# Optimization experiments

Measured on AMD Instinct MI355X. Metric: run time of the kernel, lower is better.

The kernel has to match this reference:

```python
import jax, jax.numpy as jnp
import numpy as np
import math

B, N, D, H, BS = 1, 2048, 1024, 16, 256  # batch, seq, d_model, heads, block_size


def setup_inputs() -> dict:
    key = jax.random.key(0)
    ks = jax.random.split(key, 8)
    s = 0.02  # init scale for projection weights
    return {
        "x": jax.random.normal(ks[0], (B, N, D), jnp.float32),
        "distance_bias": jax.random.uniform(ks[1], (N, N), dtype=jnp.float32),
        "Wq": jax.random.normal(ks[2], (D, D), jnp.float32) * s,
        "bq": jnp.zeros((D,), jnp.float32),
        "Wk": jax.random.normal(ks[3], (D, D), jnp.float32) * s,
        "bk": jnp.zeros((D,), jnp.float32),
        "Wv": jax.random.normal(ks[4], (D, D), jnp.float32) * s,
        "bv": jnp.zeros((D,), jnp.float32),
        "Wo": jax.random.normal(ks[5], (D, D), jnp.float32) * s,
        "bo": jnp.zeros((D,), jnp.float32),
    }


def reference(x, distance_bias, Wq, bq, Wk, bk, Wv, bv, Wo, bo):
    Bm, Nm, Dm = x.shape
    dk = Dm // H
    scale = 1.0 / math.sqrt(dk)
    nb = Nm // BS  # number of blocks along sequence

    def proj(W, b):
        # torch Linear: x @ W.T + b, then split heads -> [B, H, N, dk]
        return (x @ W.T + b).reshape(Bm, Nm, H, dk).transpose(0, 2, 1, 3)

    Q, K, V = proj(Wq, bq), proj(Wk, bk), proj(Wv, bv)

    # scores with toroidal bias subtracted (matches `scores - bias_block`)
    scores = jnp.einsum('bhqd,bhkd->bhqk', Q, K) * scale - distance_bias[None, None]
    # view as [B, H, n_qblk, BS, n_kblk, BS] and softmax PER (q-block, k-block)
    s6 = scores.reshape(Bm, H, nb, BS, nb, BS)
    w = jax.nn.softmax(s6, axis=-1)  # softmax over keys within each kv block

    Vb = V.reshape(Bm, H, nb, BS, dk)
    # sum over all kv blocks of (per-block softmax) @ V_block
    num = jnp.einsum('bhqsnk,bhnkd->bhqsd', w, Vb)  # [B,H,nb,BS,dk]
    # accumulated normalizer = sum of per-block softmax weights over all kv blocks
    norm = jnp.sum(w, axis=(4, 5))  # [B,H,nb,BS]
    O = num / (norm[..., None] + 1e-8)

    O = O.reshape(Bm, H, Nm, dk).transpose(0, 2, 1, 3).reshape(Bm, Nm, Dm)
    return O @ Wo.T + bo
```

## Files before the change

### kernel.cpp

```cpp
#include <hip/hip_runtime.h>
#include <hip/hip_fp16.h>

typedef _Float16 half8 __attribute__((ext_vector_type(8)));
typedef _Float16 half4v __attribute__((ext_vector_type(4)));
typedef float f32x4 __attribute__((ext_vector_type(4)));

#define NSEQ 2048
#define DMOD 1024
#define NHEAD 16
#define DK 64

#define GLOAD_LDS16(gp, lp) __builtin_amdgcn_global_load_lds(                 \
    (const __attribute__((address_space(1))) void*)(gp),                      \
    (__attribute__((address_space(3))) void*)(lp), 16, 0, 0)

#define WAIT_VM(n) (0xF70 | (n))


__global__ __launch_bounds__(256) void cast_pack(
    const float* __restrict__ x, const float* __restrict__ wq,
    const float* __restrict__ wk, const float* __restrict__ wv,
    const float* __restrict__ wo, _Float16* __restrict__ dst)
{
    const int w = blockIdx.x * 4 + (threadIdx.x >> 6);
    const int ln = threadIdx.x & 63, m = ln & 15, qd = ln >> 4;
    const float* src; _Float16* d; int loc;
    if (w < 4096) { src = x; d = dst; loc = w; }
    else {
        const int w2 = w - 4096, mat = w2 >> 11;
        loc = w2 & 2047;
        src = mat == 0 ? wq : mat == 1 ? wk : mat == 2 ? wv : wo;
        d = dst + 2097152 + mat * 1048576;
    }
    const int st = loc >> 5, kc = loc & 31;
    const float* p = src + (size_t)(st * 16 + m) * 1024 + kc * 32 + qd * 8;
    float4 a = *(const float4*)p, b = *(const float4*)(p + 4);
    half8 h;
    h[0] = (_Float16)a.x; h[1] = (_Float16)a.y; h[2] = (_Float16)a.z; h[3] = (_Float16)a.w;
    h[4] = (_Float16)b.x; h[5] = (_Float16)b.y; h[6] = (_Float16)b.z; h[7] = (_Float16)b.w;
    *(half8*)(d + (size_t)(loc * 64 + ln) * 8) = h;
}

__global__ __launch_bounds__(256) void cvt_bias(
    const float* __restrict__ src, _Float16* __restrict__ dst)
{
    int i = (blockIdx.x * 256 + threadIdx.x) * 4;
    float4 v = *(const float4*)(src + i);
    half4v h;
    h[0] = (_Float16)v.x; h[1] = (_Float16)v.y;
    h[2] = (_Float16)v.z; h[3] = (_Float16)v.w;
    *(half4v*)(dst + i) = h;
}

__global__ __launch_bounds__(256) void combine(
    const _Float16* __restrict__ a, const _Float16* __restrict__ b,
    _Float16* __restrict__ o)
{
    int i = (blockIdx.x * 256 + threadIdx.x) * 8;
    half8 x = *(const half8*)(a + i);
    half8 y = *(const half8*)(b + i);
    half8 r;
#pragma unroll
    for (int j = 0; j < 8; ++j) r[j] = (_Float16)((float)x[j] + (float)y[j]);
    *(half8*)(o + i) = r;
}

template<int BM, int BN, int MODE>
__global__ __launch_bounds__(256) void tgemm(
    const _Float16* __restrict__ A,
    const _Float16* __restrict__ W0, const _Float16* __restrict__ W1,
    const _Float16* __restrict__ W2,
    const float* __restrict__ b0, const float* __restrict__ b1,
    const float* __restrict__ b2,
    _Float16* __restrict__ oQ, _Float16* __restrict__ oK,
    _Float16* __restrict__ oV, float* __restrict__ oF)
{
    constexpr int MT = BM / 32, NT = BN / 32;
    constexpr int NA = BM / 64, NB = BN / 64;
    __shared__ _Float16 sA[3 * BM * 32];
    __shared__ _Float16 sB[3 * BN * 32];
    const int tid = threadIdx.x, wv = tid >> 6, ln = tid & 63;
    const int m = ln & 15, qd = ln >> 4;
    const int row0 = blockIdx.x * BM;

    int sel = 0, colbase;
    const _Float16* W; const float* bias;
    if constexpr (MODE == 0) {
        sel = blockIdx.y >> 3;
        colbase = (blockIdx.y & 7) * BN;
        W = sel == 0 ? W0 : sel == 1 ? W1 : W2;
        bias = sel == 0 ? b0 : sel == 1 ? b1 : b2;
    } else {
        colbase = blockIdx.y * BN;
        W = W0; bias = b0;
    }
    const int wr = wv >> 1, wc = wv & 1;

    f32x4 acc[MT][NT];
#pragma unroll
    for (int i = 0; i < MT; ++i)
#pragma unroll
        for (int j = 0; j < NT; ++j) acc[i][j] = (f32x4){0.f, 0.f, 0.f, 0.f};

    auto stage = [&](int kc, int b) {
        _Float16* dA = sA + b * (BM * 32);
        _Float16* dB = sB + b * (BN * 32);
#pragma unroll
        for (int ra = 0; ra < NA; ++ra) {
            const int st = ra * 4 + wv;
            GLOAD_LDS16(A + ((size_t)((row0 >> 4) + st) * 32 + kc) * 512 + ln * 8,
                        dA + st * 512);
        }
#pragma unroll
        for (int rb = 0; rb < NB; ++rb) {
            const int st = rb * 4 + wv;
            GLOAD_LDS16(W + ((size_t)((colbase >> 4) + st) * 32 + kc) * 512 + ln * 8,
                        dB + st * 512);
        }
    };
    auto step = [&](int b) {
        const _Float16* cA = sA + b * (BM * 32);
        const _Float16* cB = sB + b * (BN * 32);
        half8 af[MT], bf[NT];
#pragma unroll
        for (int i = 0; i < MT; ++i)
            af[i] = *(const half8*)(cA + ((wr * MT + i) * 64 + ln) * 8);
#pragma unroll
        for (int j = 0; j < NT; ++j)
            bf[j] = *(const half8*)(cB + ((wc * NT + j) * 64 + ln) * 8);
#pragma unroll
        for (int i = 0; i < MT; ++i)
#pragma unroll
            for (int j = 0; j < NT; ++j)
                acc[i][j] = __builtin_amdgcn_mfma_f32_16x16x32_f16(af[i], bf[j], acc[i][j], 0, 0, 0);
    };

    stage(0, 0);
    stage(1, 1);
#pragma unroll
    for (int kc = 0; kc < 31; ++kc) {
        __builtin_amdgcn_s_waitcnt(WAIT_VM(NA + NB));
        __builtin_amdgcn_s_barrier();
        if (kc < 30) stage(kc + 2, (kc + 2) % 3);
        step(kc % 3);
    }
    __builtin_amdgcn_s_waitcnt(WAIT_VM(0));
    __builtin_amdgcn_s_barrier();
    step(1);

#pragma unroll
    for (int j = 0; j < NT; ++j) {
        const int col = colbase + wc * (BN / 2) + j * 16 + m;
        const float bv = bias[col];
#pragma unroll
        for (int i = 0; i < MT; ++i) {
            const int crow0 = row0 + wr * (BM / 2) + i * 16 + qd * 4;
            if constexpr (MODE == 1) {
#pragma unroll
                for (int r = 0; r < 4; ++r)
                    oF[(size_t)(crow0 + r) * DMOD + col] = acc[i][j][r] + bv;
            } else {
                const int h = col >> 6, d = col & 63;
                if (sel == 0) {
#pragma unroll
                    for (int r = 0; r < 4; ++r)
                        oQ[h * (NSEQ * DK) + (crow0 + r) * DK + d] =
                            (_Float16)((acc[i][j][r] + bv) * 0.125f);
                } else if (sel == 1) {
#pragma unroll
                    for (int r = 0; r < 4; ++r) {
                        const int n = crow0 + r;
                        oK[(size_t)(((h * 16 + (n >> 7)) * 16
                                     + ((n >> 4) & 7) * 2 + (d >> 5)) * 64
                                    + (n & 15) + 16 * ((d >> 3) & 3)) * 8
                           + (d & 7)] = (_Float16)(acc[i][j][r] + bv);
                    }
                } else {
                    half4v hv;
#pragma unroll
                    for (int r = 0; r < 4; ++r) hv[r] = (_Float16)(acc[i][j][r] + bv);
                    const int n0 = crow0;
                    *(half4v*)(oV + (size_t)(((h * 16 + (n0 >> 7)) * 16
                                              + ((n0 >> 5) & 3) * 4 + ((d >> 4) & 3)) * 64
                                             + (d & 15) + 16 * ((n0 >> 3) & 3)) * 8
                               + (n0 & 7)) = hv;
                }
            }
        }
    }
}

__global__ __launch_bounds__(256, 2) void attn(
    const _Float16* __restrict__ Q, const _Float16* __restrict__ Kt,
    const _Float16* __restrict__ Vt, const _Float16* __restrict__ bias_h,
    _Float16* __restrict__ Op)
{
    __shared__ _Float16 sK[8192];
    __shared__ _Float16 sV[8192];
    __shared__ _Float16 sP[16384];
    const int tid = threadIdx.x, wv = tid >> 6, ln = tid & 63;
    const int m = ln & 15, qd = ln >> 4;
    const int h = blockIdx.x;
    const int q0w = blockIdx.y * 128 + wv * 32;
    const int kvb = blockIdx.z * 8;
    const _Float16* Qh = Q + h * (NSEQ * DK);
    const _Float16* Kh = Kt + h * (NSEQ * DK) + kvb * 8192;
    const _Float16* Vh = Vt + h * (NSEQ * DK) + kvb * 8192;
    const _Float16* brow0 = bias_h + (size_t)(q0w + m) * NSEQ + kvb * 128;
    const _Float16* brow1 = bias_h + (size_t)(q0w + 16 + m) * NSEQ + kvb * 128;

    half8 qf[2][2];
#pragma unroll
    for (int u = 0; u < 2; ++u) {
        qf[u][0] = *(const half8*)(Qh + (q0w + u * 16 + m) * DK + qd * 8);
        qf[u][1] = *(const half8*)(Qh + (q0w + u * 16 + m) * DK + 32 + qd * 8);
    }

    f32x4 oacc[2][4], oU[2][4];
#pragma unroll
    for (int u = 0; u < 2; ++u)
#pragma unroll
        for (int v = 0; v < 4; ++v) {
            oacc[u][v] = (f32x4){0.f, 0.f, 0.f, 0.f};
            oU[u][v]   = (f32x4){0.f, 0.f, 0.f, 0.f};
        }
    float bsum[2] = {0.f, 0.f};

    for (int ls = 0; ls < 8; ++ls) {
        if (ls) __syncthreads();
#pragma unroll
        for (int j = 0; j < 4; ++j) {
            const int f = j * 4 + wv;
            GLOAD_LDS16(Kh + ls * 8192 + f * 512 + ln * 8, sK + f * 512);
            GLOAD_LDS16(Vh + ls * 8192 + f * 512 + ln * 8, sV + f * 512);
        }
        half4v bcur[2][8];
#pragma unroll
        for (int t = 0; t < 8; ++t) {
            bcur[0][t] = *(const half4v*)(brow0 + ls * 128 + t * 16 + qd * 4);
            bcur[1][t] = *(const half4v*)(brow1 + ls * 128 + t * 16 + qd * 4);
        }
        __syncthreads();

#pragma unroll
        for (int t = 0; t < 8; ++t) {
            half8 kf0 = *(const half8*)(sK + ((t * 2 + 0) * 64 + ln) * 8);
            half8 kf1 = *(const half8*)(sK + ((t * 2 + 1) * 64 + ln) * 8);
#pragma unroll
            for (int u = 0; u < 2; ++u) {
                f32x4 s = {0.f, 0.f, 0.f, 0.f};
                s = __builtin_amdgcn_mfma_f32_16x16x32_f16(kf0, qf[u][0], s, 0, 0, 0);
                s = __builtin_amdgcn_mfma_f32_16x16x32_f16(kf1, qf[u][1], s, 0, 0, 0);
                float p0 = __expf(s[0] - (float)bcur[u][t][0]);
                float p1 = __expf(s[1] - (float)bcur[u][t][1]);
                float p2 = __expf(s[2] - (float)bcur[u][t][2]);
                float p3 = __expf(s[3] - (float)bcur[u][t][3]);
                bsum[u] += (p0 + p1) + (p2 + p3);
                half4v ph;
                ph[0] = (_Float16)p0; ph[1] = (_Float16)p1;
                ph[2] = (_Float16)p2; ph[3] = (_Float16)p3;
                *(half4v*)(sP + wv * 4096 + u * 2048 + (t >> 1) * 512
                           + (((t & 1) * 2 + (qd >> 1)) * 16 + m) * 8
                           + (qd & 1) * 4) = ph;
            }
        }

#pragma unroll
        for (int kk = 0; kk < 4; ++kk) {
            half8 pa0 = *(const half8*)(sP + wv * 4096 + kk * 512 + ln * 8);
            half8 pa1 = *(const half8*)(sP + wv * 4096 + 2048 + kk * 512 + ln * 8);
#pragma unroll
            for (int vt = 0; vt < 4; ++vt) {
                half8 vb = *(const half8*)(sV + ((kk * 4 + vt) * 64 + ln) * 8);
                oU[0][vt] = __builtin_amdgcn_mfma_f32_16x16x32_f16(pa0, vb, oU[0][vt], 0, 0, 0);
                oU[1][vt] = __builtin_amdgcn_mfma_f32_16x16x32_f16(pa1, vb, oU[1][vt], 0, 0, 0);
            }
        }

        if (ls & 1) {
#pragma unroll
            for (int u = 0; u < 2; ++u) {
                float s2 = bsum[u];
                s2 += __shfl_xor(s2, 16, 64);
                s2 += __shfl_xor(s2, 32, 64);
                float inv = 1.0f / (8.0f * s2);
                float iv[4];
#pragma unroll
                for (int r = 0; r < 4; ++r) iv[r] = __shfl(inv, qd * 4 + r, 64);
#pragma unroll
                for (int vt = 0; vt < 4; ++vt) {
#pragma unroll
                    for (int r = 0; r < 4; ++r) oacc[u][vt][r] += iv[r] * oU[u][vt][r];
                    oU[u][vt] = (f32x4){0.f, 0.f, 0.f, 0.f};
                }
                bsum[u] = 0.f;
            }
        }
    }

    _Float16* Opz = Op + (size_t)blockIdx.z * 2097152;
#pragma unroll
    for (int u = 0; u < 2; ++u) {
        const int st = (q0w >> 4) + u;
#pragma unroll
        for (int vt = 0; vt < 4; ++vt) {
            const int d = h * 64 + vt * 16 + m;
            _Float16* base = Opz + (size_t)(st * 32 + (d >> 5)) * 512
                             + ((d >> 3) & 3) * 128 + (d & 7);
#pragma unroll
            for (int r = 0; r < 4; ++r)
                base[(qd * 4 + r) * 8] = (_Float16)oacc[u][vt][r];
        }
    }
}

extern "C" void kernel_launch(void* const* d_in, const int* in_sizes, int n_in,
                              void* d_out, int out_size, void* d_ws, size_t ws_size,
                              hipStream_t stream)
{
    const float* x  = (const float*)d_in[0];
    const float* db = (const float*)d_in[1];
    const float* Wq = (const float*)d_in[2];
    const float* bq = (const float*)d_in[3];
    const float* Wk = (const float*)d_in[4];
    const float* bk = (const float*)d_in[5];
    const float* Wv = (const float*)d_in[6];
    const float* bv = (const float*)d_in[7];
    const float* Wo = (const float*)d_in[8];
    const float* bo = (const float*)d_in[9];
    float* out = (float*)d_out;

    _Float16* ws  = (_Float16*)d_ws;
    _Float16* xh  = ws;
    _Float16* wqh = xh  + 2097152;
    _Float16* wkh = wqh + 1048576;
    _Float16* wvh = wkh + 1048576;
    _Float16* woh = wvh + 1048576;
    _Float16* Qb  = woh + 1048576;
    _Float16* Kb  = Qb  + 2097152;
    _Float16* Vtb = Kb  + 2097152;
    _Float16* Oh0 = Vtb + 2097152;
    _Float16* Oh1 = Oh0 + 2097152;
    _Float16* bh  = ws;

    cast_pack<<<3072, 256, 0, stream>>>(x, Wq, Wk, Wv, Wo, xh);

    tgemm<128, 128, 0><<<dim3(16, 24), 256, 0, stream>>>(
        xh, wqh, wkh, wvh, bq, bk, bv, Qb, Kb, Vtb, nullptr);

    cvt_bias<<<4096, 256, 0, stream>>>(db, bh);

    attn<<<dim3(NHEAD, NSEQ / 128, 2), 256, 0, stream>>>(Qb, Kb, Vtb, bh, Oh0);

    combine<<<1024, 256, 0, stream>>>(Oh0, Oh1, Oh0);

    tgemm<64, 128, 1><<<dim3(32, 8), 256, 0, stream>>>(
        Oh0, woh, nullptr, nullptr, bo, nullptr, nullptr,
        nullptr, nullptr, nullptr, out);
}
```

Before: 186.3 us.

## Load MFMA fragments directly from global memory instead of LDS staging

Removes the LDS staging (global_load_lds with triple buffering and barriers) from both the projection GEMM and the attention kernel. Operand fragments are now read straight from global memory into registers, with register double-buffering in the GEMM. The cast_pack layout is changed so each lane's global read matches the fragment it needs. This drops barriers and LDS traffic, but the data reuse across waves that LDS provided is lost, so each wave re-reads its tiles through the caches and global traffic goes up.

```diff
diff --git a/kernel.cpp b/kernel.cpp
--- a/kernel.cpp
+++ b/kernel.cpp
@@ -10,12 +10,6 @@
 #define NHEAD 16
 #define DK 64
 
-#define GLOAD_LDS16(gp, lp) __builtin_amdgcn_global_load_lds(                 \
-    (const __attribute__((address_space(1))) void*)(gp),                      \
-    (__attribute__((address_space(3))) void*)(lp), 16, 0, 0)
-
-#define WAIT_VM(n) (0xF70 | (n))
-
 
 __global__ __launch_bounds__(256) void cast_pack(
     const float* __restrict__ x, const float* __restrict__ wq,
@@ -23,7 +17,8 @@
     const float* __restrict__ wo, _Float16* __restrict__ dst)
 {
     const int w = blockIdx.x * 4 + (threadIdx.x >> 6);
-    const int ln = threadIdx.x & 63, m = ln & 15, qd = ln >> 4;
+    const int ln = threadIdx.x & 63;
+    const int r = ln >> 2, q4 = ln & 3;
     const float* src; _Float16* d; int loc;
     if (w < 4096) { src = x; d = dst; loc = w; }
     else {
@@ -33,12 +28,12 @@
         d = dst + 2097152 + mat * 1048576;
     }
     const int st = loc >> 5, kc = loc & 31;
-    const float* p = src + (size_t)(st * 16 + m) * 1024 + kc * 32 + qd * 8;
+    const float* p = src + (size_t)(st * 16 + r) * 1024 + kc * 32 + q4 * 8;
     float4 a = *(const float4*)p, b = *(const float4*)(p + 4);
     half8 h;
     h[0] = (_Float16)a.x; h[1] = (_Float16)a.y; h[2] = (_Float16)a.z; h[3] = (_Float16)a.w;
     h[4] = (_Float16)b.x; h[5] = (_Float16)b.y; h[6] = (_Float16)b.z; h[7] = (_Float16)b.w;
-    *(half8*)(d + (size_t)(loc * 64 + ln) * 8) = h;
+    *(half8*)(d + (size_t)(loc * 64 + r + 16 * q4) * 8) = h;
 }
 
 __global__ __launch_bounds__(256) void cvt_bias(
@@ -76,9 +71,6 @@
     _Float16* __restrict__ oV, float* __restrict__ oF)
 {
     constexpr int MT = BM / 32, NT = BN / 32;
-    constexpr int NA = BM / 64, NB = BN / 64;
-    __shared__ _Float16 sA[3 * BM * 32];
-    __shared__ _Float16 sB[3 * BN * 32];
     const int tid = threadIdx.x, wv = tid >> 6, ln = tid & 63;
     const int m = ln & 15, qd = ln >> 4;
     const int row0 = blockIdx.x * BM;
@@ -95,6 +87,8 @@
         W = W0; bias = b0;
     }
     const int wr = wv >> 1, wc = wv & 1;
+    const size_t rb0 = (size_t)(row0 >> 4) + wr * MT;
+    const size_t cb0 = (size_t)(colbase >> 4) + wc * NT;
 
     f32x4 acc[MT][NT];
 #pragma unroll
@@ -102,51 +96,31 @@
 #pragma unroll
         for (int j = 0; j < NT; ++j) acc[i][j] = (f32x4){0.f, 0.f, 0.f, 0.f};
 
-    auto stage = [&](int kc, int b) {
-        _Float16* dA = sA + b * (BM * 32);
-        _Float16* dB = sB + b * (BN * 32);
-#pragma unroll
-        for (int ra = 0; ra < NA; ++ra) {
-            const int st = ra * 4 + wv;
-            GLOAD_LDS16(A + ((size_t)((row0 >> 4) + st) * 32 + kc) * 512 + ln * 8,
-                        dA + st * 512);
-        }
-#pragma unroll
-        for (int rb = 0; rb < NB; ++rb) {
-            const int st = rb * 4 + wv;
-            GLOAD_LDS16(W + ((size_t)((colbase >> 4) + st) * 32 + kc) * 512 + ln * 8,
-                        dB + st * 512);
-        }
-    };
-    auto step = [&](int b) {
-        const _Float16* cA = sA + b * (BM * 32);
-        const _Float16* cB = sB + b * (BN * 32);
-        half8 af[MT], bf[NT];
+    half8 fa[2][MT], fb[2][NT];
+#pragma unroll
+    for (int i = 0; i < MT; ++i)
+        fa[0][i] = *(const half8*)(A + ((rb0 + i) * 32 + 0) * 512 + ln * 8);
+#pragma unroll
+    for (int j = 0; j < NT; ++j)
+        fb[0][j] = *(const half8*)(W + ((cb0 + j) * 32 + 0) * 512 + ln * 8);
+
+#pragma unroll
+    for (int kc = 0; kc < 32; ++kc) {
+        const int cur = kc & 1, nxt = cur ^ 1;
+        if (kc < 31) {
+#pragma unroll
+            for (int i = 0; i < MT; ++i)
+                fa[nxt][i] = *(const half8*)(A + ((rb0 + i) * 32 + kc + 1) * 512 + ln * 8);
+#pragma unroll
+            for (int j = 0; j < NT; ++j)
+                fb[nxt][j] = *(const half8*)(W + ((cb0 + j) * 32 + kc + 1) * 512 + ln * 8);
+        }
 #pragma unroll
         for (int i = 0; i < MT; ++i)
-            af[i] = *(const half8*)(cA + ((wr * MT + i) * 64 + ln) * 8);
-#pragma unroll
-        for (int j = 0; j < NT; ++j)
-            bf[j] = *(const half8*)(cB + ((wc * NT + j) * 64 + ln) * 8);
-#pragma unroll
-        for (int i = 0; i < MT; ++i)
 #pragma unroll
             for (int j = 0; j < NT; ++j)
-                acc[i][j] = __builtin_amdgcn_mfma_f32_16x16x32_f16(af[i], bf[j], acc[i][j], 0, 0, 0);
-    };
-
-    stage(0, 0);
-    stage(1, 1);
-#pragma unroll
-    for (int kc = 0; kc < 31; ++kc) {
-        __builtin_amdgcn_s_waitcnt(WAIT_VM(NA + NB));
-        __builtin_amdgcn_s_barrier();
-        if (kc < 30) stage(kc + 2, (kc + 2) % 3);
-        step(kc % 3);
-    }
-    __builtin_amdgcn_s_waitcnt(WAIT_VM(0));
-    __builtin_amdgcn_s_barrier();
-    step(1);
+                acc[i][j] = __builtin_amdgcn_mfma_f32_16x16x32_f16(fa[cur][i], fb[cur][j], acc[i][j], 0, 0, 0);
+    }
 
 #pragma unroll
     for (int j = 0; j < NT; ++j) {
@@ -195,8 +169,6 @@
     const _Float16* __restrict__ Vt, const _Float16* __restrict__ bias_h,
     _Float16* __restrict__ Op)
 {
-    __shared__ _Float16 sK[8192];
-    __shared__ _Float16 sV[8192];
     __shared__ _Float16 sP[16384];
     const int tid = threadIdx.x, wv = tid >> 6, ln = tid & 63;
     const int m = ln & 15, qd = ln >> 4;
@@ -226,26 +198,21 @@
         }
     float bsum[2] = {0.f, 0.f};
 
+#pragma unroll
     for (int ls = 0; ls < 8; ++ls) {
-        if (ls) __syncthreads();
-#pragma unroll
-        for (int j = 0; j < 4; ++j) {
-            const int f = j * 4 + wv;
-            GLOAD_LDS16(Kh + ls * 8192 + f * 512 + ln * 8, sK + f * 512);
-            GLOAD_LDS16(Vh + ls * 8192 + f * 512 + ln * 8, sV + f * 512);
-        }
+        const _Float16* kS = Kh + ls * 8192;
+        const _Float16* vS = Vh + ls * 8192;
         half4v bcur[2][8];
 #pragma unroll
         for (int t = 0; t < 8; ++t) {
             bcur[0][t] = *(const half4v*)(brow0 + ls * 128 + t * 16 + qd * 4);
             bcur[1][t] = *(const half4v*)(brow1 + ls * 128 + t * 16 + qd * 4);
         }
-        __syncthreads();
 
 #pragma unroll
         for (int t = 0; t < 8; ++t) {
-            half8 kf0 = *(const half8*)(sK + ((t * 2 + 0) * 64 + ln) * 8);
-            half8 kf1 = *(const half8*)(sK + ((t * 2 + 1) * 64 + ln) * 8);
+            half8 kf0 = *(const half8*)(kS + ((t * 2 + 0) * 64 + ln) * 8);
+            half8 kf1 = *(const half8*)(kS + ((t * 2 + 1) * 64 + ln) * 8);
 #pragma unroll
             for (int u = 0; u < 2; ++u) {
                 f32x4 s = {0.f, 0.f, 0.f, 0.f};
@@ -271,7 +238,7 @@
             half8 pa1 = *(const half8*)(sP + wv * 4096 + 2048 + kk * 512 + ln * 8);
 #pragma unroll
             for (int vt = 0; vt < 4; ++vt) {
-                half8 vb = *(const half8*)(sV + ((kk * 4 + vt) * 64 + ln) * 8);
+                half8 vb = *(const half8*)(vS + ((kk * 4 + vt) * 64 + ln) * 8);
                 oU[0][vt] = __builtin_amdgcn_mfma_f32_16x16x32_f16(pa0, vb, oU[0][vt], 0, 0, 0);
                 oU[1][vt] = __builtin_amdgcn_mfma_f32_16x16x32_f16(pa1, vb, oU[1][vt], 0, 0, 0);
             }
```

Result: slower. 240.8 us (+29.2%).
